# Kernel tuning notes

Hardware: AMD Instinct MI355X
Metric: run time of the kernel (lower is better)

## Reference

```python
import jax, jax.numpy as jnp
import numpy as np

DELTA_T = 0.01


def setup_inputs() -> dict:
    key = jax.random.key(0)
    k1, k2, k3, k4, k5 = jax.random.split(key, 5)
    B, T, D = 4096, 256, 64
    s = 1.0 / np.sqrt(D)
    return {
        "x": jax.random.normal(k1, (B, T, D), dtype=jnp.float32),
        "W1": jax.random.normal(k2, (D, D), dtype=jnp.float32) * s,
        "b1": jax.random.normal(k3, (D,), dtype=jnp.float32) * s,
        "W2": jax.random.normal(k4, (D, D), dtype=jnp.float32) * s,
        "b2": jax.random.normal(k5, (D,), dtype=jnp.float32) * s,
    }


def _step(y, W1, b1, W2, b2, dt):
    # y: [B, D]; parameterization MLP -> (mu, omega) per eigen-pair
    B, D = y.shape
    ne = D // 2
    p = jnp.tanh(y @ W1.T + b1) @ W2.T + b2          # [B, D]
    mu, omega = jnp.moveaxis(p.reshape(B, ne, 2), -1, 0)  # each [B, ne]
    e = jnp.exp(dt * mu)
    c = jnp.cos(dt * omega)
    s = jnp.sin(dt * omega)
    yp = y.reshape(B, ne, 2)
    y0, y1 = yp[..., 0], yp[..., 1]
    # block-diagonal K per pair: [[c*e, -s*e], [s*e, -c*e]] (note -c, faithful to source)
    n0 = e * (c * y0 - s * y1)
    n1 = e * (s * y0 - c * y1)
    return jnp.stack([n0, n1], axis=-1).reshape(B, D)


def reference(x, W1, b1, W2, b2):
    dt = jnp.float32(DELTA_T)
    y0 = x[:, 0, :]

    def scan_step(y, _):
        y_new = _step(y, W1, b1, W2, b2, dt)
        return y_new, y_new

    _, Y = jax.lax.scan(scan_step, y0, None, length=x.shape[1])
    return jnp.transpose(Y, (1, 0, 2))  # [B, T, D]
```

## Files before the change

### kernel.cpp

```cpp
#include <hip/hip_runtime.h>


#define T_STEPS 256
#define DD 64
#define DT 0.01f

typedef __attribute__((ext_vector_type(8))) short short8;
typedef __attribute__((ext_vector_type(4))) float f32x4;

#define MFMA_BF16(a, b, c) __builtin_amdgcn_mfma_f32_16x16x32_bf16((a), (b), (c), 0, 0, 0)

static __device__ __forceinline__ short bf16_rne(float f) {
    unsigned u = __float_as_uint(f);
    u += 0x7FFFu + ((u >> 16) & 1u);
    return (short)(u >> 16);
}
static __device__ __forceinline__ float bf16_f32(short s) {
    return __uint_as_float(((unsigned)(unsigned short)s) << 16);
}

__global__ __launch_bounds__(256, 1) void koopman_mfma(
    const float* __restrict__ x,
    const float* __restrict__ W1, const float* __restrict__ b1,
    const float* __restrict__ W2, const float* __restrict__ b2,
    float* __restrict__ out)
{
    __shared__ short y_hi[16 * DD], y_lo[16 * DD];
    __shared__ short h_hi[16 * DD], h_lo[16 * DD];

    const int tid   = threadIdx.x;
    const int w     = tid >> 6;
    const int lane  = tid & 63;
    const int m     = lane & 15;
    const int g     = lane >> 4;
    const int row0  = g << 2;
    const int b0    = blockIdx.x << 4;
    const int dglob = (w << 4) + m;
    const bool even = ((lane & 1) == 0);

    short8 w1h[2], w1l[2], w2h[2], w2l[2];
    #pragma unroll
    for (int kt = 0; kt < 2; ++kt) {
        const float* p1 = W1 + (size_t)dglob * DD + (kt << 5) + (g << 3);
        const float* p2 = W2 + (size_t)dglob * DD + (kt << 5) + (g << 3);
        #pragma unroll
        for (int e = 0; e < 8; ++e) {
            float v1 = p1[e];
            short h1 = bf16_rne(v1);
            w1h[kt][e] = h1;
            w1l[kt][e] = bf16_rne(v1 - bf16_f32(h1));
            float v2 = p2[e];
            short h2 = bf16_rne(v2);
            w2h[kt][e] = h2;
            w2l[kt][e] = bf16_rne(v2 - bf16_f32(h2));
        }
    }
    const float b1r = b1[dglob];
    const float b2r = b2[dglob];

    float yv[4];
    size_t obase[4];
    #pragma unroll
    for (int r = 0; r < 4; ++r) {
        int row = row0 + r;
        yv[r] = x[((size_t)(b0 + row) * T_STEPS) * DD + dglob];
        obase[r] = ((size_t)(b0 + row) * T_STEPS) * DD + dglob;
    }

    #pragma unroll
    for (int r = 0; r < 4; ++r) {
        int row  = row0 + r;
        int byte = ((row << 7) + (dglob << 1)) ^ ((row & 7) << 4);
        short hs = bf16_rne(yv[r]);
        *(short*)((char*)y_hi + byte) = hs;
        *(short*)((char*)y_lo + byte) = bf16_rne(yv[r] - bf16_f32(hs));
    }
    __syncthreads();

    auto ldfrag = [&](const short* base, int kt) -> short8 {
        int d0   = (kt << 5) + (g << 3);
        int byte = ((m << 7) + (d0 << 1)) ^ ((m & 7) << 4);
        return *(const short8*)((const char*)base + byte);
    };

    for (int t = 0; t < T_STEPS; ++t) {
        short8 ah0 = ldfrag(y_hi, 0), al0 = ldfrag(y_lo, 0);
        short8 ah1 = ldfrag(y_hi, 1), al1 = ldfrag(y_lo, 1);
        f32x4 acc0 = {0.f, 0.f, 0.f, 0.f};
        f32x4 acc1 = {0.f, 0.f, 0.f, 0.f};
        acc0 = MFMA_BF16(ah0, w1h[0], acc0);
        acc1 = MFMA_BF16(ah1, w1h[1], acc1);
        acc0 = MFMA_BF16(al0, w1h[0], acc0);
        acc1 = MFMA_BF16(al1, w1h[1], acc1);
        acc0 = MFMA_BF16(ah0, w1l[0], acc0);
        acc1 = MFMA_BF16(ah1, w1l[1], acc1);

        #pragma unroll
        for (int r = 0; r < 4; ++r) {
            float a  = acc0[r] + acc1[r] + b1r;
            float ex = __expf(2.0f * a);
            float th = 1.0f - __fdividef(2.0f, ex + 1.0f);
            int row  = row0 + r;
            int byte = ((row << 7) + (dglob << 1)) ^ ((row & 7) << 4);
            short hs = bf16_rne(th);
            *(short*)((char*)h_hi + byte) = hs;
            *(short*)((char*)h_lo + byte) = bf16_rne(th - bf16_f32(hs));
        }
        __syncthreads();

        ah0 = ldfrag(h_hi, 0); al0 = ldfrag(h_lo, 0);
        ah1 = ldfrag(h_hi, 1); al1 = ldfrag(h_lo, 1);
        f32x4 pc0 = {0.f, 0.f, 0.f, 0.f};
        f32x4 pc1 = {0.f, 0.f, 0.f, 0.f};
        pc0 = MFMA_BF16(ah0, w2h[0], pc0);
        pc1 = MFMA_BF16(ah1, w2h[1], pc1);
        pc0 = MFMA_BF16(al0, w2h[0], pc0);
        pc1 = MFMA_BF16(al1, w2h[1], pc1);
        pc0 = MFMA_BF16(ah0, w2l[0], pc0);
        pc1 = MFMA_BF16(ah1, w2l[1], pc1);

        #pragma unroll
        for (int r = 0; r < 4; ++r) {
            float p   = pc0[r] + pc1[r] + b2r;
            float p_o = __shfl_xor(p, 1, 64);
            float y_o = __shfl_xor(yv[r], 1, 64);
            float mu  = even ? p    : p_o;
            float om  = even ? p_o  : p;
            float yy0 = even ? yv[r] : y_o;
            float yy1 = even ? y_o   : yv[r];
            float ev  = __expf(DT * mu);
            float c   = __cosf(DT * om);
            float s   = __sinf(DT * om);
            float n = even ? ev * (c * yy0 - s * yy1)
                           : ev * (s * yy0 - c * yy1);
            yv[r] = n;
            out[obase[r] + ((size_t)t << 6)] = n;

            int row  = row0 + r;
            int byte = ((row << 7) + (dglob << 1)) ^ ((row & 7) << 4);
            short hs = bf16_rne(n);
            *(short*)((char*)y_hi + byte) = hs;
            *(short*)((char*)y_lo + byte) = bf16_rne(n - bf16_f32(hs));
        }
        __syncthreads();
    }
}

extern "C" void kernel_launch(void* const* d_in, const int* in_sizes, int n_in,
                              void* d_out, int out_size, void* d_ws, size_t ws_size,
                              hipStream_t stream) {
    const float* x  = (const float*)d_in[0];
    const float* W1 = (const float*)d_in[1];
    const float* b1 = (const float*)d_in[2];
    const float* W2 = (const float*)d_in[3];
    const float* b2 = (const float*)d_in[4];
    float* out = (float*)d_out;

    dim3 grid(4096 / 16);
    dim3 block(256);
    koopman_mfma<<<grid, block, 0, stream>>>(x, W1, b1, W2, b2, out);
}
```

Baseline: 571.1 us.

## Halve rows per block, double occupancy, replace transcendentals with polynomials

Each block now handles 8 batch rows instead of 16, so the grid doubles to 512 blocks. The upper half of the MFMA rows is zero-padded and its stores are masked, and launch bounds now allow two blocks per CU. The serial recurrence gets more parallel blocks at the cost of MFMA work wasted on padding rows. It also replaces exp/sin/cos with short Taylor polynomials, which is valid because dt*p is small, and uses truncation for the bf16 high part. LDS addresses and 32-bit output offsets are precomputed to cut per-step integer work.

```diff
diff --git a/kernel.cpp b/kernel.cpp
--- a/kernel.cpp
+++ b/kernel.cpp
@@ -4,6 +4,7 @@
 #define T_STEPS 256
 #define DD 64
 #define DT 0.01f
+#define ROWS 8
 
 typedef __attribute__((ext_vector_type(8))) short short8;
 typedef __attribute__((ext_vector_type(4))) float f32x4;
@@ -15,11 +16,14 @@
     u += 0x7FFFu + ((u >> 16) & 1u);
     return (short)(u >> 16);
 }
+static __device__ __forceinline__ short bf16_trunc(float f) {
+    return (short)(__float_as_uint(f) >> 16);
+}
 static __device__ __forceinline__ float bf16_f32(short s) {
     return __uint_as_float(((unsigned)(unsigned short)s) << 16);
 }
 
-__global__ __launch_bounds__(256, 1) void koopman_mfma(
+__global__ __launch_bounds__(256, 2) void koopman_mfma(
     const float* __restrict__ x,
     const float* __restrict__ W1, const float* __restrict__ b1,
     const float* __restrict__ W2, const float* __restrict__ b2,
@@ -34,9 +38,10 @@
     const int m     = lane & 15;
     const int g     = lane >> 4;
     const int row0  = g << 2;
-    const int b0    = blockIdx.x << 4;
+    const int b0    = blockIdx.x * ROWS;
     const int dglob = (w << 4) + m;
-    const bool even = ((lane & 1) == 0);
+    const bool even   = ((lane & 1) == 0);
+    const bool gvalid = (g < 2);
 
     short8 w1h[2], w1l[2], w2h[2], w2l[2];
     #pragma unroll
@@ -58,34 +63,40 @@
     const float b1r = b1[dglob];
     const float b2r = b2[dglob];
 
-    float yv[4];
-    size_t obase[4];
-    #pragma unroll
-    for (int r = 0; r < 4; ++r) {
-        int row = row0 + r;
-        yv[r] = x[((size_t)(b0 + row) * T_STEPS) * DD + dglob];
-        obase[r] = ((size_t)(b0 + row) * T_STEPS) * DD + dglob;
-    }
-
+    int wbyte[4];
     #pragma unroll
     for (int r = 0; r < 4; ++r) {
         int row  = row0 + r;
-        int byte = ((row << 7) + (dglob << 1)) ^ ((row & 7) << 4);
-        short hs = bf16_rne(yv[r]);
-        *(short*)((char*)y_hi + byte) = hs;
-        *(short*)((char*)y_lo + byte) = bf16_rne(yv[r] - bf16_f32(hs));
+        wbyte[r] = ((row << 7) + (dglob << 1)) ^ ((row & 7) << 4);
+    }
+    int rbyte[2];
+    #pragma unroll
+    for (int kt = 0; kt < 2; ++kt) {
+        int d0    = (kt << 5) + (g << 3);
+        rbyte[kt] = ((m << 7) + (d0 << 1)) ^ ((m & 7) << 4);
+    }
+
+    float yv[4];
+    unsigned obase[4];
+    #pragma unroll
+    for (int r = 0; r < 4; ++r) {
+        int row  = row0 + r;
+        yv[r]    = gvalid ? x[((size_t)(b0 + row) * T_STEPS) * DD + dglob] : 0.0f;
+        obase[r] = gvalid ? ((unsigned)(b0 + row) * T_STEPS * DD + dglob) : 0u;
+    }
+    #pragma unroll
+    for (int r = 0; r < 4; ++r) {
+        short hs = bf16_trunc(yv[r]);
+        *(short*)((char*)y_hi + wbyte[r]) = hs;
+        *(short*)((char*)y_lo + wbyte[r]) = bf16_rne(yv[r] - bf16_f32(hs));
     }
     __syncthreads();
 
-    auto ldfrag = [&](const short* base, int kt) -> short8 {
-        int d0   = (kt << 5) + (g << 3);
-        int byte = ((m << 7) + (d0 << 1)) ^ ((m & 7) << 4);
-        return *(const short8*)((const char*)base + byte);
-    };
-
     for (int t = 0; t < T_STEPS; ++t) {
-        short8 ah0 = ldfrag(y_hi, 0), al0 = ldfrag(y_lo, 0);
-        short8 ah1 = ldfrag(y_hi, 1), al1 = ldfrag(y_lo, 1);
+        short8 ah0 = *(const short8*)((const char*)y_hi + rbyte[0]);
+        short8 al0 = *(const short8*)((const char*)y_lo + rbyte[0]);
+        short8 ah1 = *(const short8*)((const char*)y_hi + rbyte[1]);
+        short8 al1 = *(const short8*)((const char*)y_lo + rbyte[1]);
         f32x4 acc0 = {0.f, 0.f, 0.f, 0.f};
         f32x4 acc1 = {0.f, 0.f, 0.f, 0.f};
         acc0 = MFMA_BF16(ah0, w1h[0], acc0);
@@ -100,16 +111,16 @@
             float a  = acc0[r] + acc1[r] + b1r;
             float ex = __expf(2.0f * a);
             float th = 1.0f - __fdividef(2.0f, ex + 1.0f);
-            int row  = row0 + r;
-            int byte = ((row << 7) + (dglob << 1)) ^ ((row & 7) << 4);
-            short hs = bf16_rne(th);
-            *(short*)((char*)h_hi + byte) = hs;
-            *(short*)((char*)h_lo + byte) = bf16_rne(th - bf16_f32(hs));
+            short hs = bf16_trunc(th);
+            *(short*)((char*)h_hi + wbyte[r]) = hs;
+            *(short*)((char*)h_lo + wbyte[r]) = bf16_rne(th - bf16_f32(hs));
         }
         __syncthreads();
 
-        ah0 = ldfrag(h_hi, 0); al0 = ldfrag(h_lo, 0);
-        ah1 = ldfrag(h_hi, 1); al1 = ldfrag(h_lo, 1);
+        ah0 = *(const short8*)((const char*)h_hi + rbyte[0]);
+        al0 = *(const short8*)((const char*)h_lo + rbyte[0]);
+        ah1 = *(const short8*)((const char*)h_hi + rbyte[1]);
+        al1 = *(const short8*)((const char*)h_lo + rbyte[1]);
         f32x4 pc0 = {0.f, 0.f, 0.f, 0.f};
         f32x4 pc1 = {0.f, 0.f, 0.f, 0.f};
         pc0 = MFMA_BF16(ah0, w2h[0], pc0);
@@ -124,23 +135,20 @@
             float p   = pc0[r] + pc1[r] + b2r;
             float p_o = __shfl_xor(p, 1, 64);
             float y_o = __shfl_xor(yv[r], 1, 64);
-            float mu  = even ? p    : p_o;
-            float om  = even ? p_o  : p;
-            float yy0 = even ? yv[r] : y_o;
-            float yy1 = even ? y_o   : yv[r];
-            float ev  = __expf(DT * mu);
-            float c   = __cosf(DT * om);
-            float s   = __sinf(DT * om);
-            float n = even ? ev * (c * yy0 - s * yy1)
-                           : ev * (s * yy0 - c * yy1);
+            float xm  = DT * (even ? p   : p_o);
+            float xo  = DT * (even ? p_o : p);
+            float e   = fmaf(xm, fmaf(xm, fmaf(xm, fmaf(xm, 1.f/24.f, 1.f/6.f), 0.5f), 1.f), 1.f);
+            float z   = xo * xo;
+            float c   = fmaf(z, fmaf(z, fmaf(z, -1.f/720.f, 1.f/24.f), -0.5f), 1.f);
+            float s   = xo * fmaf(z, fmaf(z, fmaf(z, -1.f/5040.f, 1.f/120.f), -1.f/6.f), 1.f);
+            float u   = fmaf(s, y_o, -(c * yv[r]));
+            float es  = even ? -e : e;
+            float n   = es * u;
             yv[r] = n;
-            out[obase[r] + ((size_t)t << 6)] = n;
-
-            int row  = row0 + r;
-            int byte = ((row << 7) + (dglob << 1)) ^ ((row & 7) << 4);
-            short hs = bf16_rne(n);
-            *(short*)((char*)y_hi + byte) = hs;
-            *(short*)((char*)y_lo + byte) = bf16_rne(n - bf16_f32(hs));
+            if (gvalid) out[obase[r] + (unsigned)(t << 6)] = n;
+            short hs = bf16_trunc(n);
+            *(short*)((char*)y_hi + wbyte[r]) = hs;
+            *(short*)((char*)y_lo + wbyte[r]) = bf16_rne(n - bf16_f32(hs));
         }
         __syncthreads();
     }
@@ -156,7 +164,7 @@
     const float* b2 = (const float*)d_in[4];
     float* out = (float*)d_out;
 
-    dim3 grid(4096 / 16);
+    dim3 grid(4096 / ROWS);
     dim3 block(256);
     koopman_mfma<<<grid, block, 0, stream>>>(x, W1, b1, W2, b2, out);
 }
```

New measurement: 626.1 us. +9.6%, slower.
